# Kernel optimization log

Hardware: AMD Instinct MI355X
Metric: run time of the kernel (lower is better)

## Reference

```python
import jax, jax.numpy as jnp
import numpy as np

N_NODES = 100000
N_EDGES = 600000
H = 128


def setup_inputs() -> dict:
    key = jax.random.key(0)
    ks = jax.random.split(key, 8)
    x = jax.random.normal(ks[0], (N_NODES, H), dtype=jnp.float32)
    edge_index = jax.random.randint(ks[1], (2, N_EDGES), 0, N_NODES, dtype=jnp.int64)
    edge_attr = jax.random.normal(ks[2], (N_EDGES, H), dtype=jnp.float32)
    # node_mlp_2 params; Linear init ~ U(-1/sqrt(fan_in), 1/sqrt(fan_in)) approximated with scaled normal
    W1 = jax.random.normal(ks[3], (2 * H, 2 * H), dtype=jnp.float32) / np.sqrt(2 * H)
    b1 = jnp.zeros((2 * H,), dtype=jnp.float32)
    gamma = jnp.ones((2 * H,), dtype=jnp.float32)
    beta = jnp.zeros((2 * H,), dtype=jnp.float32)
    prelu_a = jnp.full((1,), 0.25, dtype=jnp.float32)  # PReLU default init
    W2 = jax.random.normal(ks[4], (2 * H, H), dtype=jnp.float32) / np.sqrt(2 * H)
    b2 = jnp.zeros((H,), dtype=jnp.float32)
    return {"x": x, "edge_index": edge_index, "edge_attr": edge_attr,
            "W1": W1, "b1": b1, "gamma": gamma, "beta": beta,
            "prelu_a": prelu_a, "W2": W2, "b2": b2}


def reference(x, edge_index, edge_attr, W1, b1, gamma, beta, prelu_a, W2, b2):
    n = x.shape[0]
    col = edge_index[1]
    # scatter_mean(edge_attr, col, dim=0, dim_size=n): sum / count, 0 for empty segments
    summed = jax.ops.segment_sum(edge_attr, col, num_segments=n)  # [N, H]
    cnt = jax.ops.segment_sum(jnp.ones((edge_attr.shape[0],), edge_attr.dtype), col, num_segments=n)
    agg = summed / jnp.maximum(cnt, 1.0)[:, None]
    h = jnp.concatenate([x, agg], axis=1)  # [N, 2H]
    h = h @ W1 + b1
    # LayerNorm over last dim, eps=1e-5
    mu = jnp.mean(h, axis=-1, keepdims=True)
    var = jnp.mean(jnp.square(h - mu), axis=-1, keepdims=True)
    h = (h - mu) * jax.lax.rsqrt(var + 1e-5) * gamma + beta
    # PReLU with single shared parameter
    h = jnp.where(h >= 0, h, prelu_a[0] * h)
    return h @ W2 + b2
```

## Files before the change

kernel.cpp:

```cpp
#include <hip/hip_runtime.h>

#define NNODES 100000
#define NPAD   100032
#define NEDGES 600000
#define HDIM   128
#define H2     256
#define NB_SCAN 391

typedef __attribute__((ext_vector_type(8))) short short8;
typedef __attribute__((ext_vector_type(4))) float f32x4;
typedef __attribute__((ext_vector_type(2))) float f32x2;

static __device__ __forceinline__ ushort f32_to_bf16(float f) {
    union { float f; uint u; } c; c.f = f;
    uint u = c.u;
    return (ushort)((u + 0x7fffu + ((u >> 16) & 1u)) >> 16);
}

__device__ __forceinline__ void gload_lds16(const ushort* g, ushort* l) {
    __builtin_amdgcn_global_load_lds(
        (const __attribute__((address_space(1))) void*)g,
        (__attribute__((address_space(3))) void*)l,
        16, 0, 0);
}

__device__ __forceinline__ void pack_one(
    const float* __restrict__ W, ushort* __restrict__ Wp, int ncols, int id)
{
    int l  = id & 63;
    int ks = (id >> 6) & 7;
    int nt = id >> 9;
    int colc = nt * 16 + (l & 15);
    int kb   = ks * 32 + (l >> 4) * 8;
    short8 v;
#pragma unroll
    for (int j = 0; j < 8; ++j)
        v[j] = (short)f32_to_bf16(W[(size_t)(kb + j) * ncols + colc]);
    *(short8*)&Wp[(size_t)id * 8] = v;
}

__global__ __launch_bounds__(256) void preamble(
    int* __restrict__ deg,
    const float* __restrict__ W1, const float* __restrict__ W2,
    ushort* __restrict__ W1p, ushort* __restrict__ W2p)
{
    int id = blockIdx.x * 256 + threadIdx.x;
    if (id < 16 * 8 * 64)            pack_one(W1, W1p, H2,   id);
    else if (id < 24 * 8 * 64)       pack_one(W2, W2p, HDIM, id - 16 * 8 * 64);
    int z = id - 24 * 8 * 64;
    if (z >= 0 && z < NNODES) deg[z] = 0;
}

__global__ __launch_bounds__(256) void deg_count(
    const int* __restrict__ col, int* __restrict__ deg)
{
    int e = blockIdx.x * 256 + threadIdx.x;
    if (e < NEDGES) atomicAdd(&deg[col[e]], 1);
}

__global__ __launch_bounds__(256) void scan1(
    const int* __restrict__ deg, int* __restrict__ excl, int* __restrict__ bsum)
{
    __shared__ int s[256];
    int tid = threadIdx.x;
    int i = blockIdx.x * 256 + tid;
    int v = (i < NNODES) ? deg[i] : 0;
    s[tid] = v;
    __syncthreads();
    for (int off = 1; off < 256; off <<= 1) {
        int tv = (tid >= off) ? s[tid - off] : 0;
        __syncthreads();
        s[tid] += tv;
        __syncthreads();
    }
    if (i < NNODES) excl[i] = s[tid] - v;
    if (tid == 255) bsum[blockIdx.x] = s[255];
}

__global__ __launch_bounds__(512) void scan2(int* __restrict__ bsum)
{
    __shared__ int s[512];
    int t = threadIdx.x;
    int v = (t < NB_SCAN) ? bsum[t] : 0;
    s[t] = v;
    __syncthreads();
    for (int off = 1; off < 512; off <<= 1) {
        int u = (t >= off) ? s[t - off] : 0;
        __syncthreads();
        s[t] += u;
        __syncthreads();
    }
    if (t < NB_SCAN) bsum[t] = s[t] - v;
}

__global__ __launch_bounds__(256) void scan3(
    const int* __restrict__ excl, const int* __restrict__ bsum,
    int* __restrict__ off, int* __restrict__ cursor)
{
    int i = blockIdx.x * 256 + threadIdx.x;
    if (i < NNODES) {
        int o = excl[i] + bsum[blockIdx.x];
        off[i] = o;
        cursor[i] = o;
    }
}

__global__ __launch_bounds__(256) void fill_eid(
    const int* __restrict__ col, int* __restrict__ cursor, int* __restrict__ eid)
{
    int e = blockIdx.x * 256 + threadIdx.x;
    if (e < NEDGES) {
        int p = atomicAdd(&cursor[col[e]], 1);
        eid[p] = e;
    }
}

__global__ __launch_bounds__(256) void sort_eid(
    const int* __restrict__ off, const int* __restrict__ deg,
    int* __restrict__ eid)
{
    int n = blockIdx.x * 256 + threadIdx.x;
    if (n >= NNODES) return;
    int o = off[n], d = deg[n];
    for (int i = 1; i < d; ++i) {
        int v = eid[o + i];
        int j = i - 1;
        while (j >= 0 && eid[o + j] > v) { eid[o + j + 1] = eid[o + j]; --j; }
        eid[o + j + 1] = v;
    }
}

__global__ __launch_bounds__(256) void gather_mean(
    const float* __restrict__ x,
    const float* __restrict__ edge_attr,
    const int*   __restrict__ off,
    const int*   __restrict__ deg,
    const int*   __restrict__ eid,
    ushort*      __restrict__ hin)
{
    int wid = (blockIdx.x * 256 + threadIdx.x) >> 6;
    if (wid >= NPAD) return;
    const int l    = threadIdx.x & 63;
    const int half = l >> 5;
    const int hl   = l & 31;
    const uint sw  = ((uint)wid & 7u) << 3;

    if (wid >= NNODES) {
        ushort4 z = {0, 0, 0, 0};
        *(ushort4*)&hin[(size_t)wid * H2 + (((uint)(l * 4)) ^ sw)] = z;
        return;
    }

    {
        const int c2 = l * 2;
        f32x2 xv = __builtin_nontemporal_load(
            (const f32x2*)&x[(size_t)wid * HDIM + c2]);
        ushort2 hx;
        hx.x = f32_to_bf16(xv.x);
        hx.y = f32_to_bf16(xv.y);
        *(ushort2*)&hin[(size_t)wid * H2 + ((uint)c2 ^ sw)] = hx;
    }

    const int o  = __builtin_amdgcn_readfirstlane(off[wid]);
    const int dg = __builtin_amdgcn_readfirstlane(deg[wid]);
    const int c4 = hl * 4;

    f32x4 av = {0.f, 0.f, 0.f, 0.f};
    int p = half;
    while (p + 2 < dg) {
        int e0 = eid[o + p];
        int e1 = eid[o + p + 2];
        f32x4 v0 = __builtin_nontemporal_load(
            (const f32x4*)&edge_attr[(size_t)e0 * HDIM + c4]);
        f32x4 v1 = __builtin_nontemporal_load(
            (const f32x4*)&edge_attr[(size_t)e1 * HDIM + c4]);
        av += v0 + v1;
        p += 4;
    }
    if (p < dg) {
        int e0 = eid[o + p];
        f32x4 v0 = __builtin_nontemporal_load(
            (const f32x4*)&edge_attr[(size_t)e0 * HDIM + c4]);
        av += v0;
    }
    av.x += __shfl_xor(av.x, 32, 64);
    av.y += __shfl_xor(av.y, 32, 64);
    av.z += __shfl_xor(av.z, 32, 64);
    av.w += __shfl_xor(av.w, 32, 64);

    if (half == 0) {
        float inv = 1.0f / fmaxf((float)dg, 1.0f);
        ushort4 ha;
        ha.x = f32_to_bf16(av.x * inv);
        ha.y = f32_to_bf16(av.y * inv);
        ha.z = f32_to_bf16(av.z * inv);
        ha.w = f32_to_bf16(av.w * inv);
        *(ushort4*)&hin[(size_t)wid * H2 + ((uint)(HDIM + c4) ^ sw)] = ha;
    }
}

__global__ __launch_bounds__(512, 4) void fused_mfma(
    const ushort* __restrict__ hin,
    const ushort* __restrict__ W1p,
    const float*  __restrict__ b1,
    const float*  __restrict__ gamma,
    const float*  __restrict__ beta,
    const float*  __restrict__ prelu_a,
    const ushort* __restrict__ W2p,
    const float*  __restrict__ b2,
    float*        __restrict__ out)
{
    __shared__ ushort hbuf[64 * H2];
    __shared__ float red_s[8][64];
    __shared__ float red_q[8][64];
    __shared__ float mu_l[64];
    __shared__ float rs_l[64];

    const int t = threadIdx.x;
    const int w = t >> 6;
    const int l = t & 63;
    const int lrow = l & 15;
    const int lk   = l >> 4;
    const int row0 = blockIdx.x * 64;

    {
        const ushort* hrow = hin + (size_t)row0 * H2;
#pragma unroll
        for (int it = 0; it < 4; ++it) {
            int flat = it * 512 + t;
            gload_lds16(hrow + flat * 8, &hbuf[flat * 8]);
        }
    }
    asm volatile("s_waitcnt vmcnt(0)" ::: "memory");
    __syncthreads();

    f32x4 acc[4][2];
#pragma unroll
    for (int i = 0; i < 4; ++i)
#pragma unroll
        for (int j = 0; j < 2; ++j) acc[i][j] = (f32x4)(0.0f);

#pragma unroll
    for (int ks = 0; ks < 8; ++ks) {
        short8 a[4];
#pragma unroll
        for (int rt = 0; rt < 4; ++rt) {
            uint row = (uint)(rt * 16 + lrow);
            uint idx = ((row << 8) + (uint)(ks * 32 + lk * 8)) ^ ((row & 7u) << 3);
            a[rt] = *(const short8*)&hbuf[idx];
        }
#pragma unroll
        for (int ct = 0; ct < 2; ++ct) {
            short8 b = *(const short8*)&W1p[(size_t)(((w * 2 + ct) * 8 + ks) * 64 + l) * 8];
#pragma unroll
            for (int rt = 0; rt < 4; ++rt)
                acc[rt][ct] = __builtin_amdgcn_mfma_f32_16x16x32_bf16(
                    a[rt], b, acc[rt][ct], 0, 0, 0);
        }
    }

    float b1c[2], g1c[2], be1c[2];
#pragma unroll
    for (int ct = 0; ct < 2; ++ct) {
        int colc = w * 32 + ct * 16 + lrow;
        b1c[ct] = b1[colc]; g1c[ct] = gamma[colc]; be1c[ct] = beta[colc];
    }
#pragma unroll
    for (int rt = 0; rt < 4; ++rt)
#pragma unroll
        for (int ct = 0; ct < 2; ++ct)
#pragma unroll
            for (int r = 0; r < 4; ++r) acc[rt][ct][r] += b1c[ct];

#pragma unroll
    for (int rt = 0; rt < 4; ++rt) {
        float s[4], qq[4];
#pragma unroll
        for (int r = 0; r < 4; ++r) {
            float v0 = acc[rt][0][r], v1 = acc[rt][1][r];
            s[r]  = v0 + v1;
            qq[r] = v0 * v0 + v1 * v1;
        }
#pragma unroll
        for (int off2 = 1; off2 < 16; off2 <<= 1) {
#pragma unroll
            for (int r = 0; r < 4; ++r) {
                s[r]  += __shfl_xor(s[r],  off2, 64);
                qq[r] += __shfl_xor(qq[r], off2, 64);
            }
        }
        if (lrow == 0) {
#pragma unroll
            for (int r = 0; r < 4; ++r) {
                int row = rt * 16 + lk * 4 + r;
                red_s[w][row] = s[r];
                red_q[w][row] = qq[r];
            }
        }
    }
    __syncthreads();
    if (t < 64) {
        float s = 0.f, qq = 0.f;
#pragma unroll
        for (int ww = 0; ww < 8; ++ww) { s += red_s[ww][t]; qq += red_q[ww][t]; }
        float mu  = s * (1.0f / H2);
        float var = qq * (1.0f / H2) - mu * mu;
        mu_l[t] = mu;
        rs_l[t] = rsqrtf(var + 1e-5f);
    }
    const float ap = prelu_a[0];
    __syncthreads();

#pragma unroll
    for (int rt = 0; rt < 4; ++rt) {
#pragma unroll
        for (int r = 0; r < 4; ++r) {
            uint row = (uint)(rt * 16 + lk * 4 + r);
            float mu = mu_l[row], rs = rs_l[row];
#pragma unroll
            for (int ct = 0; ct < 2; ++ct) {
                uint colc = (uint)(w * 32 + ct * 16 + lrow);
                float v = (acc[rt][ct][r] - mu) * rs * g1c[ct] + be1c[ct];
                v = v >= 0.0f ? v : ap * v;
                uint idx = ((row << 8) + colc) ^ ((row & 7u) << 3);
                hbuf[idx] = f32_to_bf16(v);
            }
        }
    }
    __syncthreads();

    f32x4 acc2[4];
#pragma unroll
    for (int i = 0; i < 4; ++i) acc2[i] = (f32x4)(0.0f);

#pragma unroll
    for (int ks = 0; ks < 8; ++ks) {
        short8 a[4];
#pragma unroll
        for (int rt = 0; rt < 4; ++rt) {
            uint row = (uint)(rt * 16 + lrow);
            uint idx = ((row << 8) + (uint)(ks * 32 + lk * 8)) ^ ((row & 7u) << 3);
            a[rt] = *(const short8*)&hbuf[idx];
        }
        short8 b = *(const short8*)&W2p[(size_t)((w * 8 + ks) * 64 + l) * 8];
#pragma unroll
        for (int rt = 0; rt < 4; ++rt)
            acc2[rt] = __builtin_amdgcn_mfma_f32_16x16x32_bf16(
                a[rt], b, acc2[rt], 0, 0, 0);
    }

    float b2c = b2[w * 16 + lrow];
#pragma unroll
    for (int rt = 0; rt < 4; ++rt)
#pragma unroll
        for (int r = 0; r < 4; ++r) {
            int row = row0 + rt * 16 + lk * 4 + r;
            if (row < NNODES)
                out[(size_t)row * HDIM + w * 16 + lrow] = acc2[rt][r] + b2c;
        }
}

extern "C" void kernel_launch(void* const* d_in, const int* in_sizes, int n_in,
                              void* d_out, int out_size, void* d_ws, size_t ws_size,
                              hipStream_t stream)
{
    const float* x         = (const float*)d_in[0];
    const int*   ei        = (const int*)  d_in[1];
    const float* edge_attr = (const float*)d_in[2];
    const float* W1        = (const float*)d_in[3];
    const float* b1        = (const float*)d_in[4];
    const float* gamma     = (const float*)d_in[5];
    const float* beta      = (const float*)d_in[6];
    const float* prelu_a   = (const float*)d_in[7];
    const float* W2        = (const float*)d_in[8];
    const float* b2        = (const float*)d_in[9];
    float*       out       = (float*)d_out;

    int* deg    = (int*)d_ws;
    int* excl   = deg + NNODES;
    int* bsum   = excl + NNODES;
    int* off    = bsum + 512;
    int* cursor = off + NNODES;
    int* eid    = cursor + NNODES;
    ushort* W1p = (ushort*)(eid + NEDGES);
    ushort* W2p = W1p + 16 * 8 * 64 * 8;
    ushort* hin = W2p + 8 * 8 * 64 * 8;

    const int* colp = ei + NEDGES;

    preamble<<<48 + NB_SCAN, 256, 0, stream>>>(deg, W1, W2, W1p, W2p);
    deg_count<<<(NEDGES + 255) / 256, 256, 0, stream>>>(colp, deg);
    scan1<<<NB_SCAN, 256, 0, stream>>>(deg, excl, bsum);
    scan2<<<1, 512, 0, stream>>>(bsum);
    scan3<<<NB_SCAN, 256, 0, stream>>>(excl, bsum, off, cursor);
    fill_eid<<<(NEDGES + 255) / 256, 256, 0, stream>>>(colp, cursor, eid);
    sort_eid<<<NB_SCAN, 256, 0, stream>>>(off, deg, eid);

    gather_mean<<<NPAD / 4, 256, 0, stream>>>(
        x, edge_attr, off, deg, eid, hin);

    fused_mfma<<<NPAD / 64, 512, 0, stream>>>(
        hin, W1p, b1, gamma, beta, prelu_a, W2p, b2, out);
}
```

Baseline: 218.2 us.

## Double MFMA block rows to 128 and fold block-sum scan into scan3

The fused MLP kernel now processes 128 rows per block instead of 64, so each weight fragment loaded from global memory is reused across twice as many MFMA row tiles. Shared memory per block doubles to about 64KB and accumulator registers grow, which with launch_bounds(512,4) risks spills or lower occupancy. Separately, the single-block scan2 launch is removed and each scan3 block sums the preceding block totals itself, saving one kernel launch at the cost of redundant reads. NPAD grows to a multiple of 128.

```diff
diff --git a/kernel.cpp b/kernel.cpp
--- a/kernel.cpp
+++ b/kernel.cpp
@@ -1,10 +1,11 @@
 #include <hip/hip_runtime.h>
 
 #define NNODES 100000
-#define NPAD   100032
+#define NPAD   100096
 #define NEDGES 600000
 #define HDIM   128
 #define H2     256
+#define BROWS  128
 #define NB_SCAN 391
 
 typedef __attribute__((ext_vector_type(8))) short short8;
@@ -77,29 +78,23 @@
     if (tid == 255) bsum[blockIdx.x] = s[255];
 }
 
-__global__ __launch_bounds__(512) void scan2(int* __restrict__ bsum)
-{
-    __shared__ int s[512];
-    int t = threadIdx.x;
-    int v = (t < NB_SCAN) ? bsum[t] : 0;
-    s[t] = v;
-    __syncthreads();
-    for (int off = 1; off < 512; off <<= 1) {
-        int u = (t >= off) ? s[t - off] : 0;
-        __syncthreads();
-        s[t] += u;
-        __syncthreads();
-    }
-    if (t < NB_SCAN) bsum[t] = s[t] - v;
-}
-
 __global__ __launch_bounds__(256) void scan3(
     const int* __restrict__ excl, const int* __restrict__ bsum,
     int* __restrict__ off, int* __restrict__ cursor)
 {
-    int i = blockIdx.x * 256 + threadIdx.x;
+    __shared__ int wsum[4];
+    int tid = threadIdx.x;
+    int b   = blockIdx.x;
+    int partial = 0;
+    for (int i = tid; i < b; i += 256) partial += bsum[i];
+#pragma unroll
+    for (int o = 32; o; o >>= 1) partial += __shfl_xor(partial, o, 64);
+    if ((tid & 63) == 0) wsum[tid >> 6] = partial;
+    __syncthreads();
+    int base = wsum[0] + wsum[1] + wsum[2] + wsum[3];
+    int i = b * 256 + tid;
     if (i < NNODES) {
-        int o = excl[i] + bsum[blockIdx.x];
+        int o = excl[i] + base;
         off[i] = o;
         cursor[i] = o;
     }
@@ -210,23 +205,23 @@
     const float*  __restrict__ b2,
     float*        __restrict__ out)
 {
-    __shared__ ushort hbuf[64 * H2];
-    __shared__ float red_s[8][64];
-    __shared__ float red_q[8][64];
-    __shared__ float mu_l[64];
-    __shared__ float rs_l[64];
+    __shared__ ushort hbuf[BROWS * H2];
+    __shared__ float red_s[8][BROWS];
+    __shared__ float red_q[8][BROWS];
+    __shared__ float mu_l[BROWS];
+    __shared__ float rs_l[BROWS];
 
     const int t = threadIdx.x;
     const int w = t >> 6;
     const int l = t & 63;
     const int lrow = l & 15;
     const int lk   = l >> 4;
-    const int row0 = blockIdx.x * 64;
+    const int row0 = blockIdx.x * BROWS;
 
     {
         const ushort* hrow = hin + (size_t)row0 * H2;
 #pragma unroll
-        for (int it = 0; it < 4; ++it) {
+        for (int it = 0; it < 8; ++it) {
             int flat = it * 512 + t;
             gload_lds16(hrow + flat * 8, &hbuf[flat * 8]);
         }
@@ -234,17 +229,17 @@
     asm volatile("s_waitcnt vmcnt(0)" ::: "memory");
     __syncthreads();
 
-    f32x4 acc[4][2];
-#pragma unroll
-    for (int i = 0; i < 4; ++i)
+    f32x4 acc[8][2];
+#pragma unroll
+    for (int i = 0; i < 8; ++i)
 #pragma unroll
         for (int j = 0; j < 2; ++j) acc[i][j] = (f32x4)(0.0f);
 
 #pragma unroll
     for (int ks = 0; ks < 8; ++ks) {
-        short8 a[4];
-#pragma unroll
-        for (int rt = 0; rt < 4; ++rt) {
+        short8 a[8];
+#pragma unroll
+        for (int rt = 0; rt < 8; ++rt) {
             uint row = (uint)(rt * 16 + lrow);
             uint idx = ((row << 8) + (uint)(ks * 32 + lk * 8)) ^ ((row & 7u) << 3);
             a[rt] = *(const short8*)&hbuf[idx];
@@ -253,7 +248,7 @@
         for (int ct = 0; ct < 2; ++ct) {
             short8 b = *(const short8*)&W1p[(size_t)(((w * 2 + ct) * 8 + ks) * 64 + l) * 8];
 #pragma unroll
-            for (int rt = 0; rt < 4; ++rt)
+            for (int rt = 0; rt < 8; ++rt)
                 acc[rt][ct] = __builtin_amdgcn_mfma_f32_16x16x32_bf16(
                     a[rt], b, acc[rt][ct], 0, 0, 0);
         }
@@ -266,14 +261,14 @@
         b1c[ct] = b1[colc]; g1c[ct] = gamma[colc]; be1c[ct] = beta[colc];
     }
 #pragma unroll
-    for (int rt = 0; rt < 4; ++rt)
+    for (int rt = 0; rt < 8; ++rt)
 #pragma unroll
         for (int ct = 0; ct < 2; ++ct)
 #pragma unroll
             for (int r = 0; r < 4; ++r) acc[rt][ct][r] += b1c[ct];
 
 #pragma unroll
-    for (int rt = 0; rt < 4; ++rt) {
+    for (int rt = 0; rt < 8; ++rt) {
         float s[4], qq[4];
 #pragma unroll
         for (int r = 0; r < 4; ++r) {
@@ -299,7 +294,7 @@
         }
     }
     __syncthreads();
-    if (t < 64) {
+    if (t < BROWS) {
         float s = 0.f, qq = 0.f;
 #pragma unroll
         for (int ww = 0; ww < 8; ++ww) { s += red_s[ww][t]; qq += red_q[ww][t]; }
@@ -312,7 +307,7 @@
     __syncthreads();
 
 #pragma unroll
-    for (int rt = 0; rt < 4; ++rt) {
+    for (int rt = 0; rt < 8; ++rt) {
 #pragma unroll
         for (int r = 0; r < 4; ++r) {
             uint row = (uint)(rt * 16 + lk * 4 + r);
@@ -329,29 +324,29 @@
     }
     __syncthreads();
 
-    f32x4 acc2[4];
-#pragma unroll
-    for (int i = 0; i < 4; ++i) acc2[i] = (f32x4)(0.0f);
+    f32x4 acc2[8];
+#pragma unroll
+    for (int i = 0; i < 8; ++i) acc2[i] = (f32x4)(0.0f);
 
 #pragma unroll
     for (int ks = 0; ks < 8; ++ks) {
-        short8 a[4];
-#pragma unroll
-        for (int rt = 0; rt < 4; ++rt) {
+        short8 a[8];
+#pragma unroll
+        for (int rt = 0; rt < 8; ++rt) {
             uint row = (uint)(rt * 16 + lrow);
             uint idx = ((row << 8) + (uint)(ks * 32 + lk * 8)) ^ ((row & 7u) << 3);
             a[rt] = *(const short8*)&hbuf[idx];
         }
         short8 b = *(const short8*)&W2p[(size_t)((w * 8 + ks) * 64 + l) * 8];
 #pragma unroll
-        for (int rt = 0; rt < 4; ++rt)
+        for (int rt = 0; rt < 8; ++rt)
             acc2[rt] = __builtin_amdgcn_mfma_f32_16x16x32_bf16(
                 a[rt], b, acc2[rt], 0, 0, 0);
     }
 
     float b2c = b2[w * 16 + lrow];
 #pragma unroll
-    for (int rt = 0; rt < 4; ++rt)
+    for (int rt = 0; rt < 8; ++rt)
 #pragma unroll
         for (int r = 0; r < 4; ++r) {
             int row = row0 + rt * 16 + lk * 4 + r;
@@ -391,7 +386,6 @@
     preamble<<<48 + NB_SCAN, 256, 0, stream>>>(deg, W1, W2, W1p, W2p);
     deg_count<<<(NEDGES + 255) / 256, 256, 0, stream>>>(colp, deg);
     scan1<<<NB_SCAN, 256, 0, stream>>>(deg, excl, bsum);
-    scan2<<<1, 512, 0, stream>>>(bsum);
     scan3<<<NB_SCAN, 256, 0, stream>>>(excl, bsum, off, cursor);
     fill_eid<<<(NEDGES + 255) / 256, 256, 0, stream>>>(colp, cursor, eid);
     sort_eid<<<NB_SCAN, 256, 0, stream>>>(off, deg, eid);
@@ -399,6 +393,6 @@
     gather_mean<<<NPAD / 4, 256, 0, stream>>>(
         x, edge_attr, off, deg, eid, hin);
 
-    fused_mfma<<<NPAD / 64, 512, 0, stream>>>(
+    fused_mfma<<<NPAD / BROWS, 512, 0, stream>>>(
         hin, W1p, b1, gamma, beta, prelu_a, W2p, b2, out);
 }
```

Result: slower. 255.1 us (+16.9%).

## Load x directly in MFMA kernel and fold block-sum scan into scan3

Applied to the files above, without the earlier changes.

The gather kernel now writes only the bf16 mean aggregate into a compact [N,128] buffer. The fused MFMA kernel loads x in fp32, converts it to bf16 and writes both halves into swizzled LDS itself, so the bf16 copy of x no longer round-trips through global memory. The scan2 launch is removed: each scan3 block sums the preceding block totals itself. In exchange, the async global-to-LDS loads are replaced by synchronous register loads, and scan3 does redundant prefix reads of bsum.

```diff
diff --git a/kernel.cpp b/kernel.cpp
--- a/kernel.cpp
+++ b/kernel.cpp
@@ -17,13 +17,6 @@
     return (ushort)((u + 0x7fffu + ((u >> 16) & 1u)) >> 16);
 }
 
-__device__ __forceinline__ void gload_lds16(const ushort* g, ushort* l) {
-    __builtin_amdgcn_global_load_lds(
-        (const __attribute__((address_space(1))) void*)g,
-        (__attribute__((address_space(3))) void*)l,
-        16, 0, 0);
-}
-
 __device__ __forceinline__ void pack_one(
     const float* __restrict__ W, ushort* __restrict__ Wp, int ncols, int id)
 {
@@ -77,29 +70,23 @@
     if (tid == 255) bsum[blockIdx.x] = s[255];
 }
 
-__global__ __launch_bounds__(512) void scan2(int* __restrict__ bsum)
-{
-    __shared__ int s[512];
-    int t = threadIdx.x;
-    int v = (t < NB_SCAN) ? bsum[t] : 0;
-    s[t] = v;
-    __syncthreads();
-    for (int off = 1; off < 512; off <<= 1) {
-        int u = (t >= off) ? s[t - off] : 0;
-        __syncthreads();
-        s[t] += u;
-        __syncthreads();
-    }
-    if (t < NB_SCAN) bsum[t] = s[t] - v;
-}
-
 __global__ __launch_bounds__(256) void scan3(
     const int* __restrict__ excl, const int* __restrict__ bsum,
     int* __restrict__ off, int* __restrict__ cursor)
 {
-    int i = blockIdx.x * 256 + threadIdx.x;
+    __shared__ int wsum[4];
+    int tid = threadIdx.x;
+    int b   = blockIdx.x;
+    int partial = 0;
+    for (int i = tid; i < b; i += 256) partial += bsum[i];
+#pragma unroll
+    for (int o = 32; o; o >>= 1) partial += __shfl_xor(partial, o, 64);
+    if ((tid & 63) == 0) wsum[tid >> 6] = partial;
+    __syncthreads();
+    int base = wsum[0] + wsum[1] + wsum[2] + wsum[3];
+    int i = b * 256 + tid;
     if (i < NNODES) {
-        int o = excl[i] + bsum[blockIdx.x];
+        int o = excl[i] + base;
         off[i] = o;
         cursor[i] = o;
     }
@@ -131,34 +118,22 @@
 }
 
 __global__ __launch_bounds__(256) void gather_mean(
-    const float* __restrict__ x,
     const float* __restrict__ edge_attr,
     const int*   __restrict__ off,
     const int*   __restrict__ deg,
     const int*   __restrict__ eid,
-    ushort*      __restrict__ hin)
+    ushort*      __restrict__ agg)
 {
     int wid = (blockIdx.x * 256 + threadIdx.x) >> 6;
     if (wid >= NPAD) return;
     const int l    = threadIdx.x & 63;
     const int half = l >> 5;
     const int hl   = l & 31;
-    const uint sw  = ((uint)wid & 7u) << 3;
 
     if (wid >= NNODES) {
-        ushort4 z = {0, 0, 0, 0};
-        *(ushort4*)&hin[(size_t)wid * H2 + (((uint)(l * 4)) ^ sw)] = z;
+        ushort2 z = {0, 0};
+        *(ushort2*)&agg[(size_t)wid * HDIM + l * 2] = z;
         return;
-    }
-
-    {
-        const int c2 = l * 2;
-        f32x2 xv = __builtin_nontemporal_load(
-            (const f32x2*)&x[(size_t)wid * HDIM + c2]);
-        ushort2 hx;
-        hx.x = f32_to_bf16(xv.x);
-        hx.y = f32_to_bf16(xv.y);
-        *(ushort2*)&hin[(size_t)wid * H2 + ((uint)c2 ^ sw)] = hx;
     }
 
     const int o  = __builtin_amdgcn_readfirstlane(off[wid]);
@@ -195,12 +170,13 @@
         ha.y = f32_to_bf16(av.y * inv);
         ha.z = f32_to_bf16(av.z * inv);
         ha.w = f32_to_bf16(av.w * inv);
-        *(ushort4*)&hin[(size_t)wid * H2 + ((uint)(HDIM + c4) ^ sw)] = ha;
+        *(ushort4*)&agg[(size_t)wid * HDIM + c4] = ha;
     }
 }
 
 __global__ __launch_bounds__(512, 4) void fused_mfma(
-    const ushort* __restrict__ hin,
+    const float*  __restrict__ x,
+    const ushort* __restrict__ agg,
     const ushort* __restrict__ W1p,
     const float*  __restrict__ b1,
     const float*  __restrict__ gamma,
@@ -223,15 +199,30 @@
     const int lk   = l >> 4;
     const int row0 = blockIdx.x * 64;
 
-    {
-        const ushort* hrow = hin + (size_t)row0 * H2;
-#pragma unroll
-        for (int it = 0; it < 4; ++it) {
-            int flat = it * 512 + t;
-            gload_lds16(hrow + flat * 8, &hbuf[flat * 8]);
-        }
-    }
-    asm volatile("s_waitcnt vmcnt(0)" ::: "memory");
+#pragma unroll
+    for (int it = 0; it < 4; ++it) {
+        int flat = it * 512 + t;
+        int lr = flat >> 5;
+        int qc = flat & 31;
+        int row = row0 + lr;
+        float4 v = {0.f, 0.f, 0.f, 0.f};
+        if (row < NNODES)
+            v = *(const float4*)&x[(size_t)row * HDIM + qc * 4];
+        ushort4 h;
+        h.x = f32_to_bf16(v.x); h.y = f32_to_bf16(v.y);
+        h.z = f32_to_bf16(v.z); h.w = f32_to_bf16(v.w);
+        uint idx = (((uint)lr << 8) + (uint)(qc * 4)) ^ (((uint)lr & 7u) << 3);
+        *(ushort4*)&hbuf[idx] = h;
+    }
+#pragma unroll
+    for (int it = 0; it < 4; ++it) {
+        int flat = it * 512 + t;
+        int lr = flat >> 5;
+        int qc = flat & 31;
+        ushort4 v = *(const ushort4*)&agg[(size_t)(row0 + lr) * HDIM + qc * 4];
+        uint idx = (((uint)lr << 8) + (uint)(HDIM + qc * 4)) ^ (((uint)lr & 7u) << 3);
+        *(ushort4*)&hbuf[idx] = v;
+    }
     __syncthreads();
 
     f32x4 acc[4][2];
@@ -384,21 +375,20 @@
     int* eid    = cursor + NNODES;
     ushort* W1p = (ushort*)(eid + NEDGES);
     ushort* W2p = W1p + 16 * 8 * 64 * 8;
-    ushort* hin = W2p + 8 * 8 * 64 * 8;
+    ushort* agg = W2p + 8 * 8 * 64 * 8;
 
     const int* colp = ei + NEDGES;
 
     preamble<<<48 + NB_SCAN, 256, 0, stream>>>(deg, W1, W2, W1p, W2p);
     deg_count<<<(NEDGES + 255) / 256, 256, 0, stream>>>(colp, deg);
     scan1<<<NB_SCAN, 256, 0, stream>>>(deg, excl, bsum);
-    scan2<<<1, 512, 0, stream>>>(bsum);
     scan3<<<NB_SCAN, 256, 0, stream>>>(excl, bsum, off, cursor);
     fill_eid<<<(NEDGES + 255) / 256, 256, 0, stream>>>(colp, cursor, eid);
     sort_eid<<<NB_SCAN, 256, 0, stream>>>(off, deg, eid);
 
     gather_mean<<<NPAD / 4, 256, 0, stream>>>(
-        x, edge_attr, off, deg, eid, hin);
+        edge_attr, off, deg, eid, agg);
 
     fused_mfma<<<NPAD / 64, 512, 0, stream>>>(
-        hin, W1p, b1, gamma, beta, prelu_a, W2p, b2, out);
-}
+        x, agg, W1p, b1, gamma, beta, prelu_a, W2p, b2, out);
+}
```

After: 220.1 us. No clear change (+0.9%).
